# Kernel tuning notes

Measured on AMD Instinct MI355X. Metric: run time of the kernel, lower is better.

Reference implementation:

```python
import jax, jax.numpy as jnp
import numpy as np

NEIGHBOR_RATE = 0.1  # neighbor_rate init arg
LEAKY_SLOPE = 0.2
NEG_INF = -1.0e9


def setup_inputs() -> dict:
    key = jax.random.key(0)
    k1, k2, k3, k4 = jax.random.split(key, 4)
    B, N, Din, H, hd = 4, 2048, 128, 4, 32  # output_dim = H*hd = 128
    h = jax.random.normal(k1, (B, N, Din), jnp.float32)
    adj = jax.random.uniform(k2, (B, N, N), jnp.float32)
    # stacked per-head params: W[k] in [Din, hd], a[k] in [2*hd]
    w_bound = 1.0 / np.sqrt(Din)
    a_bound = 1.0 / np.sqrt(2 * hd)
    W = jax.random.uniform(k3, (H, Din, hd), jnp.float32, -w_bound, w_bound)
    a = jax.random.uniform(k4, (H, 2 * hd), jnp.float32, -a_bound, a_bound)
    return {"h": h, "adj": adj, "W": W, "a": a}


def reference(h, adj, W, a):
    B, N, _ = h.shape
    H, _, hd = W.shape
    k = int(NEIGHBOR_RATE * N)  # num_neighbors
    # Wh: [B,H,N,hd]
    Wh = jnp.einsum('bnf,hfd->bhnd', h, W)
    # cat([Wh_i, Wh_j]) @ a  ==  Wh_i @ a[:hd] + Wh_j @ a[hd:] (broadcast trick)
    s_i = jnp.einsum('bhnd,hd->bhn', Wh, a[:, :hd])
    s_j = jnp.einsum('bhnd,hd->bhn', Wh, a[:, hd:])
    e = jax.nn.leaky_relu(s_i[..., :, None] + s_j[..., None, :], LEAKY_SLOPE)  # [B,H,N,N]
    # top-k mask along last (neighbor) axis, built by scatter like torch .scatter_
    _, idx = jax.lax.top_k(e, k)  # [B,H,N,k]
    row_mask = lambda i: jnp.zeros((N,), jnp.bool_).at[i].set(True)
    mask = jax.vmap(row_mask)(idx.reshape(-1, k)).reshape(e.shape)
    masked = jnp.where(mask, e, NEG_INF)
    attn = jax.nn.softmax(masked, axis=-1) * adj[:, None]  # [B,H,N,N]
    hp = jnp.einsum('bhnm,bhmd->bhnd', attn, Wh)
    # concat heads on feature dim -> [B,N,H*hd]
    return hp.transpose(0, 2, 1, 3).reshape(B, N, H * hd)
```

## Files before the change

### kernel.cpp

```cpp
#include <hip/hip_runtime.h>
#include <hip/hip_bf16.h>
#include <cmath>

#define BB 4
#define NN 2048
#define DIN 128
#define HH 4
#define HD 32
#define KSEL 204
#define BH (BB*HH)
#define KPAD 256
#define CRPB 4

typedef __attribute__((ext_vector_type(8))) short short8;
typedef __attribute__((ext_vector_type(4))) short short4v;
typedef __attribute__((ext_vector_type(4))) float float4v;

static __device__ inline short f2bf(float x) {
    __hip_bfloat16 b = __float2bfloat16(x);
    return __builtin_bit_cast(short, b);
}

__global__ __launch_bounds__(256) void hcvt_kernel(const float* __restrict__ h,
                                                   short* __restrict__ hbf) {
    int tid = blockIdx.x * 256 + threadIdx.x;
    float4 x = ((const float4*)h)[tid];
    short4v r;
    r[0] = f2bf(x.x); r[1] = f2bf(x.y); r[2] = f2bf(x.z); r[3] = f2bf(x.w);
    *(short4v*)(hbf + (size_t)tid * 4) = r;
}

__global__ __launch_bounds__(256) void s_kernel(const float* __restrict__ h,
                                                const float* __restrict__ W,
                                                const float* __restrict__ a,
                                                float* __restrict__ si, float* __restrict__ sj) {
    int bh = blockIdx.x >> 3, chunk = blockIdx.x & 7;
    int b = bh >> 2, hh = bh & 3;
    __shared__ float w1[128], w2[128];
    int t = threadIdx.x;
    {
        int f = t & 127, half = t >> 7;
        const float* Wp = W + (size_t)hh * (DIN * HD) + f * HD;
        const float* ap = a + hh * 64 + half * 32;
        float acc = 0.f;
#pragma unroll
        for (int d = 0; d < 32; ++d) acc += Wp[d] * ap[d];
        if (half == 0) w1[f] = acc; else w2[f] = acc;
    }
    __syncthreads();
    int n = chunk * 256 + t;
    const float4* hr = (const float4*)(h + ((size_t)b * NN + n) * DIN);
    float s1 = 0.f, s2 = 0.f;
#pragma unroll 8
    for (int q = 0; q < 32; ++q) {
        float4 x = hr[q];
        s1 += x.x * w1[q*4] + x.y * w1[q*4+1] + x.z * w1[q*4+2] + x.w * w1[q*4+3];
        s2 += x.x * w2[q*4] + x.y * w2[q*4+1] + x.z * w2[q*4+2] + x.w * w2[q*4+3];
    }
    int o = bh * NN + n;
    si[o] = s1; sj[o] = s2;
}

__global__ __launch_bounds__(256) void wh_kernel(const short* __restrict__ hbf,
                                                 const float* __restrict__ W,
                                                 short* __restrict__ Whg) {
    int bh = blockIdx.x >> 4, rtile = blockIdx.x & 15;
    int b = bh >> 2, hh = bh & 3;
    __shared__ short WT[32][136];
    int t = threadIdx.x;
    for (int e = t; e < 32 * 128; e += 256) {
        int n = e >> 7, k = e & 127;
        WT[n][k] = f2bf(W[(size_t)hh * (DIN * HD) + k * HD + n]);
    }
    __syncthreads();
    int w = t >> 6, lane = t & 63, mr = lane & 15, quad = lane >> 4;
    int row_base = rtile * 128;
#pragma unroll
    for (int q = 0; q < 4; ++q) {
        int tt = w * 4 + q;
        int rt = tt >> 1, ct = tt & 1;
        int row0 = row_base + rt * 16;
        const short* hrow = hbf + ((size_t)b * NN + row0 + mr) * DIN + quad * 8;
        float4v acc = {0.f, 0.f, 0.f, 0.f};
#pragma unroll
        for (int ks = 0; ks < 4; ++ks) {
            short8 afr = *(const short8*)(hrow + ks * 32);
            short8 bfr = *(const short8*)&WT[ct * 16 + mr][ks * 32 + quad * 8];
            acc = __builtin_amdgcn_mfma_f32_16x16x32_bf16(afr, bfr, acc, 0, 0, 0);
        }
#pragma unroll
        for (int r = 0; r < 4; ++r) {
            int rowg = row0 + quad * 4 + r;
            Whg[((size_t)bh * NN + rowg) * HD + ct * 16 + mr] = f2bf(acc[r]);
        }
    }
}

__global__ __launch_bounds__(256) void select_kernel(
        const float* __restrict__ sj, const short* __restrict__ Whg,
        int* __restrict__ idxsel, float* __restrict__ sjsel,
        float* __restrict__ sjmax, short* __restrict__ Whsel) {
    int bh = blockIdx.x;
    int t = threadIdx.x, lane = t & 63, w = t >> 6;
    __shared__ float sv[NN];
    __shared__ unsigned kv[NN];
    __shared__ int hist4[4][256];
    __shared__ int binInfo[2];
    __shared__ int wtot[4];
    __shared__ int wtotg[4], wtote[4], woffg[4], woffe[4];
    __shared__ float wmax[4];
    __shared__ int idxLDS[KSEL];

    const float* s = sj + (size_t)bh * NN;
    float lmax = -1e30f;
    for (int e = t; e < NN; e += 256) {
        float x = s[e];
        sv[e] = x;
        unsigned u = __builtin_bit_cast(unsigned, x);
        kv[e] = (u & 0x80000000u) ? ~u : (u | 0x80000000u);
        lmax = fmaxf(lmax, x);
    }
#pragma unroll
    for (int off = 32; off >= 1; off >>= 1) lmax = fmaxf(lmax, __shfl_xor(lmax, off));
    if (lane == 0) wmax[w] = lmax;
    __syncthreads();
    if (t == 0) sjmax[bh] = fmaxf(fmaxf(wmax[0], wmax[1]), fmaxf(wmax[2], wmax[3]));

    unsigned prefix = 0;
    int need = KSEL;
    for (int shift = 24; shift >= 0; shift -= 8) {
        hist4[0][t] = 0; hist4[1][t] = 0; hist4[2][t] = 0; hist4[3][t] = 0;
        __syncthreads();
        unsigned hmask = (shift < 24) ? (0xFFFFFFFFu << (shift + 8)) : 0u;
        for (int e = t; e < NN; e += 256) {
            unsigned k = kv[e];
            if (((k ^ prefix) & hmask) == 0)
                atomicAdd(&hist4[w][(k >> shift) & 255], 1);
        }
        __syncthreads();
        int bb = 255 - t;
        int hv = hist4[0][bb] + hist4[1][bb] + hist4[2][bb] + hist4[3][bb];
        int sc = hv;
#pragma unroll
        for (int off = 1; off < 64; off <<= 1) {
            int u = __shfl_up(sc, off);
            if (lane >= off) sc += u;
        }
        if (lane == 63) wtot[w] = sc;
        __syncthreads();
        int woffset = 0;
#pragma unroll
        for (int i = 0; i < 4; ++i) woffset += (i < w) ? wtot[i] : 0;
        int incl = sc + woffset;
        int excl = incl - hv;
        if (incl >= need && excl < need) {
            binInfo[0] = bb;
            binInfo[1] = excl;
        }
        __syncthreads();
        prefix |= ((unsigned)binInfo[0]) << shift;
        need -= binInfo[1];
    }
    unsigned T = prefix;
    int n_gt = KSEL - need;

    int j0 = t * 8;
    unsigned kk[8];
    int cg = 0, ce = 0;
#pragma unroll
    for (int r = 0; r < 8; ++r) {
        kk[r] = kv[j0 + r];
        cg += (kk[r] > T) ? 1 : 0;
        ce += (kk[r] == T) ? 1 : 0;
    }
    int sg = cg, se = ce;
#pragma unroll
    for (int off = 1; off < 64; off <<= 1) {
        int ug = __shfl_up(sg, off), ue = __shfl_up(se, off);
        if (lane >= off) { sg += ug; se += ue; }
    }
    if (lane == 63) { wtotg[w] = sg; wtote[w] = se; }
    __syncthreads();
    if (t == 0) {
        int rg = 0, re = 0;
        for (int i = 0; i < 4; ++i) {
            woffg[i] = rg; rg += wtotg[i];
            woffe[i] = re; re += wtote[i];
        }
    }
    __syncthreads();
    int pg = woffg[w] + sg - cg;
    int te = woffe[w] + se - ce;
#pragma unroll
    for (int r = 0; r < 8; ++r) {
        int j = j0 + r;
        if (kk[r] > T) {
            idxsel[bh * KSEL + pg] = j;
            sjsel[bh * KSEL + pg] = sv[j];
            idxLDS[pg] = j;
            pg++;
        } else if (kk[r] == T) {
            if (te < need) {
                int pos = n_gt + te;
                idxsel[bh * KSEL + pos] = j;
                sjsel[bh * KSEL + pos] = sv[j];
                idxLDS[pos] = j;
            }
            te++;
        }
    }
    __syncthreads();
    for (int e = t; e < HD * KPAD; e += 256) {
        int d = e >> 8, jj = e & 255;
        short v = 0;
        if (jj < KSEL) v = Whg[((size_t)bh * NN + idxLDS[jj]) * HD + d];
        Whsel[((size_t)bh * HD + d) * KPAD + jj] = v;
    }
}

__global__ __launch_bounds__(256) void coef_kernel(
        const float* __restrict__ adj, const float* __restrict__ si,
        const int* __restrict__ idxsel, const float* __restrict__ sjsel,
        const float* __restrict__ sjmax, short* __restrict__ PS,
        float* __restrict__ invZ) {
    int b = blockIdx.x >> 9;
    int chunk = blockIdx.x & 511;
    __shared__ float adjbuf[CRPB][NN];
    __shared__ int   idxS[HH][KSEL];
    __shared__ float sjS[HH][KSEL];
    __shared__ float smaxS[HH];
    int t = threadIdx.x, w = t >> 6, lane = t & 63;
    int i0 = chunk * CRPB;
    const float* adjb = adj + (size_t)b * NN * NN;
    {
        const float4* src = (const float4*)(adjb + (size_t)i0 * NN);
        float4* dst = (float4*)adjbuf;
#pragma unroll
        for (int q = 0; q < CRPB * 2; ++q)
            dst[q * 256 + t] = src[q * 256 + t];
    }
    for (int e = t; e < HH * KSEL; e += 256) {
        int hh = e / KSEL, jj = e - hh * KSEL;
        idxS[hh][jj] = idxsel[(b * HH + hh) * KSEL + jj];
        sjS[hh][jj]  = sjsel[(b * HH + hh) * KSEL + jj];
    }
    if (t < HH) smaxS[t] = sjmax[b * HH + t];
    __syncthreads();
    int bh = b * HH + w;
    float smax = smaxS[w];
#pragma unroll
    for (int r = 0; r < CRPB; ++r) {
        const float* ab = adjbuf[r];
        int i = i0 + r;
        float siv = si[(size_t)bh * NN + i];
        float m = siv + smax;
        m = (m >= 0.f) ? m : 0.2f * m;
        float z = 0.f;
        short* prow = PS + ((size_t)bh * NN + i) * KPAD;
#pragma unroll
        for (int k = 0; k < 4; ++k) {
            int jj = k * 64 + lane;
            bool valid = jj < KSEL;
            int j = valid ? idxS[w][jj] : 0;
            float av = ab[j];
            float e = siv + (valid ? sjS[w][jj] : 0.f);
            e = (e >= 0.f) ? e : 0.2f * e;
            float c = valid ? __expf(e - m) : 0.f;
            z += c;
            prow[jj] = f2bf(c * av);
        }
#pragma unroll
        for (int off = 32; off >= 1; off >>= 1) z += __shfl_xor(z, off);
        if (lane == 0) invZ[(size_t)bh * NN + i] = 1.0f / z;
    }
}

__global__ __launch_bounds__(256) void pv_kernel(
        const short* __restrict__ PS, const short* __restrict__ Whsel,
        const float* __restrict__ invZ, float* __restrict__ out) {
    int bh = blockIdx.x >> 6, tile = blockIdx.x & 63;
    int b = bh >> 2, hh = bh & 3;
    int t = threadIdx.x, w = t >> 6, lane = t & 63;
    int mr = lane & 15, quad = lane >> 4;
    int mi = w >> 1, ni = w & 1;
    int i0 = tile * 32;
    const short* pA = PS + ((size_t)bh * NN + i0 + mi * 16 + mr) * KPAD + quad * 8;
    const short* pB = Whsel + ((size_t)bh * HD + ni * 16 + mr) * KPAD + quad * 8;
    float4v acc = {0.f, 0.f, 0.f, 0.f};
#pragma unroll
    for (int ks = 0; ks < 8; ++ks) {
        short8 afr = *(const short8*)(pA + ks * 32);
        short8 bfr = *(const short8*)(pB + ks * 32);
        acc = __builtin_amdgcn_mfma_f32_16x16x32_bf16(afr, bfr, acc, 0, 0, 0);
    }
#pragma unroll
    for (int r = 0; r < 4; ++r) {
        int i = i0 + mi * 16 + quad * 4 + r;
        int d = ni * 16 + mr;
        out[((size_t)(b * NN + i)) * (HH * HD) + hh * HD + d] =
            acc[r] * invZ[(size_t)bh * NN + i];
    }
}

extern "C" void kernel_launch(void* const* d_in, const int* in_sizes, int n_in,
                              void* d_out, int out_size, void* d_ws, size_t ws_size,
                              hipStream_t stream) {
    const float* h   = (const float*)d_in[0];
    const float* adj = (const float*)d_in[1];
    const float* W   = (const float*)d_in[2];
    const float* a   = (const float*)d_in[3];
    float* out = (float*)d_out;

    float* si     = (float*)d_ws;
    float* sj     = si + (size_t)BH * NN;
    float* invZ   = sj + (size_t)BH * NN;
    float* sjsel  = invZ + (size_t)BH * NN;
    float* sjmax  = sjsel + (size_t)BH * KSEL;
    int*   idxsel = (int*)(sjmax + 16);
    short* hbf    = (short*)(idxsel + (size_t)BH * KSEL);
    short* Whg    = hbf + (size_t)BB * NN * DIN;
    short* Whsel  = Whg + (size_t)BH * NN * HD;
    short* PS     = Whsel + (size_t)BH * HD * KPAD;

    hcvt_kernel<<<(BB * NN * DIN) / 1024, 256, 0, stream>>>(h, hbf);
    s_kernel<<<BH * 8, 256, 0, stream>>>(h, W, a, si, sj);
    wh_kernel<<<BH * 16, 256, 0, stream>>>(hbf, W, Whg);
    select_kernel<<<BH, 256, 0, stream>>>(sj, Whg, idxsel, sjsel, sjmax, Whsel);
    coef_kernel<<<BB * (NN / CRPB), 256, 0, stream>>>(adj, si, idxsel, sjsel, sjmax, PS, invZ);
    pv_kernel<<<BH * 64, 256, 0, stream>>>(PS, Whsel, invZ, out);
}
```

Before: 145.4 us.

## Fuse bf16 conversion into score kernel, widen top-k select to 1024 threads

Merges the h-to-bf16 conversion into the score kernel, removing one launch and one extra pass over h. The radix top-k select kernel now runs 1024 threads per block with keys held in registers (two per thread) and 16 per-wave histograms, to shorten this low-parallelism stage that runs only 16 blocks. The coefficient kernel pads the selected-index arrays to 256, so its branches disappear and it writes packed bf16 pairs. The cost is more barriers, a larger per-block footprint in select, and padding filled with a sentinel value.

Result: faster. 141.3 us (-2.8%).

```diff
diff --git a/kernel.cpp b/kernel.cpp
--- a/kernel.cpp
+++ b/kernel.cpp
@@ -21,23 +21,27 @@
     return __builtin_bit_cast(short, b);
 }
 
-__global__ __launch_bounds__(256) void hcvt_kernel(const float* __restrict__ h,
-                                                   short* __restrict__ hbf) {
-    int tid = blockIdx.x * 256 + threadIdx.x;
-    float4 x = ((const float4*)h)[tid];
-    short4v r;
-    r[0] = f2bf(x.x); r[1] = f2bf(x.y); r[2] = f2bf(x.z); r[3] = f2bf(x.w);
-    *(short4v*)(hbf + (size_t)tid * 4) = r;
-}
-
-__global__ __launch_bounds__(256) void s_kernel(const float* __restrict__ h,
-                                                const float* __restrict__ W,
-                                                const float* __restrict__ a,
-                                                float* __restrict__ si, float* __restrict__ sj) {
-    int bh = blockIdx.x >> 3, chunk = blockIdx.x & 7;
+__global__ __launch_bounds__(256) void hs_kernel(const float* __restrict__ h,
+                                                 const float* __restrict__ W,
+                                                 const float* __restrict__ a,
+                                                 short* __restrict__ hbf,
+                                                 float* __restrict__ si, float* __restrict__ sj) {
+    int g = blockIdx.x;
+    int bh = g >> 3, chunk = g & 7;
     int b = bh >> 2, hh = bh & 3;
+    int t = threadIdx.x;
+    {
+        const float4* src = (const float4*)h + (size_t)g * 2048;
+        short4v* dst = (short4v*)hbf + (size_t)g * 2048;
+#pragma unroll
+        for (int q = 0; q < 8; ++q) {
+            float4 x = src[q * 256 + t];
+            short4v r;
+            r[0] = f2bf(x.x); r[1] = f2bf(x.y); r[2] = f2bf(x.z); r[3] = f2bf(x.w);
+            dst[q * 256 + t] = r;
+        }
+    }
     __shared__ float w1[128], w2[128];
-    int t = threadIdx.x;
     {
         int f = t & 127, half = t >> 7;
         const float* Wp = W + (size_t)hh * (DIN * HD) + f * HD;
@@ -96,83 +100,87 @@
     }
 }
 
-__global__ __launch_bounds__(256) void select_kernel(
+__global__ __launch_bounds__(1024) void select_kernel(
         const float* __restrict__ sj, const short* __restrict__ Whg,
         int* __restrict__ idxsel, float* __restrict__ sjsel,
         float* __restrict__ sjmax, short* __restrict__ Whsel) {
     int bh = blockIdx.x;
     int t = threadIdx.x, lane = t & 63, w = t >> 6;
     __shared__ float sv[NN];
-    __shared__ unsigned kv[NN];
-    __shared__ int hist4[4][256];
+    __shared__ int hist16[16][256];
     __shared__ int binInfo[2];
     __shared__ int wtot[4];
-    __shared__ int wtotg[4], wtote[4], woffg[4], woffe[4];
-    __shared__ float wmax[4];
+    __shared__ int wtotg[16], wtote[16], woffg[16], woffe[16];
+    __shared__ float wmax[16];
     __shared__ int idxLDS[KSEL];
 
     const float* s = sj + (size_t)bh * NN;
-    float lmax = -1e30f;
-    for (int e = t; e < NN; e += 256) {
-        float x = s[e];
-        sv[e] = x;
-        unsigned u = __builtin_bit_cast(unsigned, x);
-        kv[e] = (u & 0x80000000u) ? ~u : (u | 0x80000000u);
-        lmax = fmaxf(lmax, x);
-    }
+    int j0 = t * 2;
+    float x0 = s[j0], x1 = s[j0 + 1];
+    sv[j0] = x0; sv[j0 + 1] = x1;
+    unsigned u0 = __builtin_bit_cast(unsigned, x0);
+    unsigned u1 = __builtin_bit_cast(unsigned, x1);
+    u0 = (u0 & 0x80000000u) ? ~u0 : (u0 | 0x80000000u);
+    u1 = (u1 & 0x80000000u) ? ~u1 : (u1 | 0x80000000u);
+    float lmax = fmaxf(x0, x1);
 #pragma unroll
     for (int off = 32; off >= 1; off >>= 1) lmax = fmaxf(lmax, __shfl_xor(lmax, off));
     if (lane == 0) wmax[w] = lmax;
     __syncthreads();
-    if (t == 0) sjmax[bh] = fmaxf(fmaxf(wmax[0], wmax[1]), fmaxf(wmax[2], wmax[3]));
+    if (t == 0) {
+        float m = wmax[0];
+#pragma unroll
+        for (int i = 1; i < 16; ++i) m = fmaxf(m, wmax[i]);
+        sjmax[bh] = m;
+    }
 
     unsigned prefix = 0;
     int need = KSEL;
+#pragma unroll
     for (int shift = 24; shift >= 0; shift -= 8) {
-        hist4[0][t] = 0; hist4[1][t] = 0; hist4[2][t] = 0; hist4[3][t] = 0;
+        ((int*)hist16)[t] = 0; ((int*)hist16)[t + 1024] = 0;
+        ((int*)hist16)[t + 2048] = 0; ((int*)hist16)[t + 3072] = 0;
         __syncthreads();
         unsigned hmask = (shift < 24) ? (0xFFFFFFFFu << (shift + 8)) : 0u;
-        for (int e = t; e < NN; e += 256) {
-            unsigned k = kv[e];
-            if (((k ^ prefix) & hmask) == 0)
-                atomicAdd(&hist4[w][(k >> shift) & 255], 1);
-        }
-        __syncthreads();
-        int bb = 255 - t;
-        int hv = hist4[0][bb] + hist4[1][bb] + hist4[2][bb] + hist4[3][bb];
-        int sc = hv;
-#pragma unroll
-        for (int off = 1; off < 64; off <<= 1) {
-            int u = __shfl_up(sc, off);
-            if (lane >= off) sc += u;
-        }
-        if (lane == 63) wtot[w] = sc;
-        __syncthreads();
-        int woffset = 0;
-#pragma unroll
-        for (int i = 0; i < 4; ++i) woffset += (i < w) ? wtot[i] : 0;
-        int incl = sc + woffset;
-        int excl = incl - hv;
-        if (incl >= need && excl < need) {
-            binInfo[0] = bb;
-            binInfo[1] = excl;
+        if (((u0 ^ prefix) & hmask) == 0) atomicAdd(&hist16[w][(u0 >> shift) & 255], 1);
+        if (((u1 ^ prefix) & hmask) == 0) atomicAdd(&hist16[w][(u1 >> shift) & 255], 1);
+        __syncthreads();
+        int sc = 0, hv = 0, bb = 0;
+        if (t < 256) {
+            bb = 255 - t;
+            hv = 0;
+#pragma unroll
+            for (int i = 0; i < 16; ++i) hv += hist16[i][bb];
+            sc = hv;
+#pragma unroll
+            for (int off = 1; off < 64; off <<= 1) {
+                int u = __shfl_up(sc, off);
+                if (lane >= off) sc += u;
+            }
+            if (lane == 63) wtot[w] = sc;
+        }
+        __syncthreads();
+        if (t < 256) {
+            int woffset = 0;
+#pragma unroll
+            for (int i = 0; i < 4; ++i) woffset += (i < w) ? wtot[i] : 0;
+            int incl = sc + woffset;
+            int excl = incl - hv;
+            if (incl >= need && excl < need) {
+                binInfo[0] = bb;
+                binInfo[1] = excl;
+            }
         }
         __syncthreads();
         prefix |= ((unsigned)binInfo[0]) << shift;
         need -= binInfo[1];
+        __syncthreads();
     }
     unsigned T = prefix;
     int n_gt = KSEL - need;
 
-    int j0 = t * 8;
-    unsigned kk[8];
-    int cg = 0, ce = 0;
-#pragma unroll
-    for (int r = 0; r < 8; ++r) {
-        kk[r] = kv[j0 + r];
-        cg += (kk[r] > T) ? 1 : 0;
-        ce += (kk[r] == T) ? 1 : 0;
-    }
+    int cg = (u0 > T ? 1 : 0) + (u1 > T ? 1 : 0);
+    int ce = (u0 == T ? 1 : 0) + (u1 == T ? 1 : 0);
     int sg = cg, se = ce;
 #pragma unroll
     for (int off = 1; off < 64; off <<= 1) {
@@ -183,7 +191,8 @@
     __syncthreads();
     if (t == 0) {
         int rg = 0, re = 0;
-        for (int i = 0; i < 4; ++i) {
+#pragma unroll
+        for (int i = 0; i < 16; ++i) {
             woffg[i] = rg; rg += wtotg[i];
             woffe[i] = re; re += wtote[i];
         }
@@ -191,26 +200,29 @@
     __syncthreads();
     int pg = woffg[w] + sg - cg;
     int te = woffe[w] + se - ce;
-#pragma unroll
-    for (int r = 0; r < 8; ++r) {
-        int j = j0 + r;
-        if (kk[r] > T) {
-            idxsel[bh * KSEL + pg] = j;
-            sjsel[bh * KSEL + pg] = sv[j];
-            idxLDS[pg] = j;
-            pg++;
-        } else if (kk[r] == T) {
-            if (te < need) {
-                int pos = n_gt + te;
-                idxsel[bh * KSEL + pos] = j;
-                sjsel[bh * KSEL + pos] = sv[j];
-                idxLDS[pos] = j;
+    {
+        unsigned kk[2] = {u0, u1};
+#pragma unroll
+        for (int r = 0; r < 2; ++r) {
+            int j = j0 + r;
+            if (kk[r] > T) {
+                idxsel[bh * KSEL + pg] = j;
+                sjsel[bh * KSEL + pg] = sv[j];
+                idxLDS[pg] = j;
+                pg++;
+            } else if (kk[r] == T) {
+                if (te < need) {
+                    int pos = n_gt + te;
+                    idxsel[bh * KSEL + pos] = j;
+                    sjsel[bh * KSEL + pos] = sv[j];
+                    idxLDS[pos] = j;
+                }
+                te++;
             }
-            te++;
-        }
-    }
-    __syncthreads();
-    for (int e = t; e < HD * KPAD; e += 256) {
+        }
+    }
+    __syncthreads();
+    for (int e = t; e < HD * KPAD; e += 1024) {
         int d = e >> 8, jj = e & 255;
         short v = 0;
         if (jj < KSEL) v = Whg[((size_t)bh * NN + idxLDS[jj]) * HD + d];
@@ -226,8 +238,8 @@
     int b = blockIdx.x >> 9;
     int chunk = blockIdx.x & 511;
     __shared__ float adjbuf[CRPB][NN];
-    __shared__ int   idxS[HH][KSEL];
-    __shared__ float sjS[HH][KSEL];
+    __shared__ int   idxS[HH][KPAD];
+    __shared__ float sjS[HH][KPAD];
     __shared__ float smaxS[HH];
     int t = threadIdx.x, w = t >> 6, lane = t & 63;
     int i0 = chunk * CRPB;
@@ -239,10 +251,11 @@
         for (int q = 0; q < CRPB * 2; ++q)
             dst[q * 256 + t] = src[q * 256 + t];
     }
-    for (int e = t; e < HH * KSEL; e += 256) {
-        int hh = e / KSEL, jj = e - hh * KSEL;
-        idxS[hh][jj] = idxsel[(b * HH + hh) * KSEL + jj];
-        sjS[hh][jj]  = sjsel[(b * HH + hh) * KSEL + jj];
+    for (int e = t; e < HH * KPAD; e += 256) {
+        int hh = e >> 8, jj = e & 255;
+        bool v = jj < KSEL;
+        idxS[hh][jj] = v ? idxsel[(b * HH + hh) * KSEL + jj] : 0;
+        sjS[hh][jj]  = v ? sjsel[(b * HH + hh) * KSEL + jj] : -1e30f;
     }
     if (t < HH) smaxS[t] = sjmax[b * HH + t];
     __syncthreads();
@@ -258,16 +271,21 @@
         float z = 0.f;
         short* prow = PS + ((size_t)bh * NN + i) * KPAD;
 #pragma unroll
-        for (int k = 0; k < 4; ++k) {
-            int jj = k * 64 + lane;
-            bool valid = jj < KSEL;
-            int j = valid ? idxS[w][jj] : 0;
-            float av = ab[j];
-            float e = siv + (valid ? sjS[w][jj] : 0.f);
-            e = (e >= 0.f) ? e : 0.2f * e;
-            float c = valid ? __expf(e - m) : 0.f;
-            z += c;
-            prow[jj] = f2bf(c * av);
+        for (int k = 0; k < 2; ++k) {
+            int jj = k * 128 + lane * 2;
+            int ja = idxS[w][jj], jb = idxS[w][jj + 1];
+            float ava = ab[ja], avb = ab[jb];
+            float ea = siv + sjS[w][jj];
+            float eb = siv + sjS[w][jj + 1];
+            ea = (ea >= 0.f) ? ea : 0.2f * ea;
+            eb = (eb >= 0.f) ? eb : 0.2f * eb;
+            float ca = __expf(ea - m);
+            float cb = __expf(eb - m);
+            z += ca + cb;
+            short2 p;
+            p.x = f2bf(ca * ava);
+            p.y = f2bf(cb * avb);
+            *(short2*)&prow[jj] = p;
         }
 #pragma unroll
         for (int off = 32; off >= 1; off >>= 1) z += __shfl_xor(z, off);
@@ -322,10 +340,9 @@
     short* Whsel  = Whg + (size_t)BH * NN * HD;
     short* PS     = Whsel + (size_t)BH * HD * KPAD;
 
-    hcvt_kernel<<<(BB * NN * DIN) / 1024, 256, 0, stream>>>(h, hbf);
-    s_kernel<<<BH * 8, 256, 0, stream>>>(h, W, a, si, sj);
+    hs_kernel<<<BH * 8, 256, 0, stream>>>(h, W, a, hbf, si, sj);
     wh_kernel<<<BH * 16, 256, 0, stream>>>(hbf, W, Whg);
-    select_kernel<<<BH, 256, 0, stream>>>(sj, Whg, idxsel, sjsel, sjmax, Whsel);
+    select_kernel<<<BH, 1024, 0, stream>>>(sj, Whg, idxsel, sjsel, sjmax, Whsel);
     coef_kernel<<<BB * (NN / CRPB), 256, 0, stream>>>(adj, si, idxsel, sjsel, sjmax, PS, invZ);
     pv_kernel<<<BH * 64, 256, 0, stream>>>(PS, Whsel, invZ, out);
 }
```
